# Performance work log

Measured on AMD Instinct MI355X. Metric: run time of the kernel, lower is better.

Reference implementation:

```python
import jax, jax.numpy as jnp
import numpy as np

L = 32768   # sequence length
H = 256     # dim_ssm_io
P = 128     # effective state dim = dim_ssm_state // 2 (conj_sym=True)
DT_MIN, DT_MAX = 0.001, 0.1


def setup_inputs() -> dict:
    key = jax.random.key(0)
    kB, kC, kD, kstep, ku = jax.random.split(key, 5)
    n = jnp.arange(P, dtype=jnp.float32)
    # s4d_inv initialization: Lambda = -0.5 + 1j * (P/pi) * (P/(2n+1) - 1)
    Lambda_re = -0.5 * jnp.ones((P,), dtype=jnp.float32)
    Lambda_im = (P / np.pi) * (P / (2.0 * n + 1.0) - 1.0)
    # lecun_normal over fan_in, then / sqrt(2) for conj_sym real/imag split
    B = jax.random.normal(kB, (P, H, 2), dtype=jnp.float32) / jnp.sqrt(2.0 * H)
    C = jax.random.normal(kC, (H, P, 2), dtype=jnp.float32) / jnp.sqrt(2.0 * P)
    D = jax.random.normal(kD, (H,), dtype=jnp.float32)
    log_step = (jax.random.uniform(kstep, (P,), dtype=jnp.float32)
                * (jnp.log(DT_MAX) - jnp.log(DT_MIN)) + jnp.log(DT_MIN))
    input_sequence = jax.random.normal(ku, (L, H), dtype=jnp.float32)
    return {
        "Lambda_re": Lambda_re, "Lambda_im": Lambda_im,
        "B": B, "C": C, "D": D, "log_step": log_step,
        "input_sequence": input_sequence,
    }


def reference(Lambda_re, Lambda_im, B, C, D, log_step, input_sequence):
    # assemble complex params (conj_sym path)
    Lam = Lambda_re + 1j * Lambda_im              # (P,)
    B_tilde = B[..., 0] + 1j * B[..., 1]          # (P, H)
    C_tilde = C[..., 0] + 1j * C[..., 1]          # (H, P)
    step = jnp.exp(log_step)                      # (P,)  step_rescale = 1.0
    # ZOH discretization
    Lambda_bar = jnp.exp(Lam * step)              # (P,)
    B_bar = ((Lambda_bar - 1.0) / Lam)[:, None] * B_tilde  # (P, H)
    # input projection: Bu[l] = B_bar @ u[l]
    Bu = jnp.einsum("lh,ph->lp", input_sequence.astype(B_bar.dtype), B_bar)  # (L, P)
    Lam_elems = jnp.broadcast_to(Lambda_bar, (input_sequence.shape[0], Lambda_bar.shape[0]))

    def lin_op(q_i, q_j):
        A_i, b_i = q_i
        A_j, b_j = q_j
        return (A_j * A_i, A_j * b_i + b_j)

    _, xs = jax.lax.associative_scan(lin_op, (Lam_elems, Bu))  # (L, P) complex
    # output projection with conj symmetry: 2 * Re(C_tilde @ x)
    ys = 2.0 * jnp.einsum("lp,hp->lh", xs, C_tilde).real       # (L, H)
    return ys + D * input_sequence
```

## Files before the change

### kernel.cpp

```cpp
#include <hip/hip_runtime.h>
#include <math.h>

#define L_SEQ   32768
#define H_DIM   256
#define P_DIM   128
#define P2      256
#define NBLK    512
#define ROWS    64
#define TPB     512
#define NSEG    64
#define CPS     8

#define WS_LB    0
#define WS_A64   256
#define WS_A512  512
#define WS_COEF  768
#define WS_APOW  1024
#define WS_E     17408
#define WS_CB    148480
#define WS_PACKS 279552
#define WS_XS    410624
#define WS_S     8799232
#define WS_SC    8815616

typedef __attribute__((ext_vector_type(8))) short short8;
typedef __attribute__((ext_vector_type(4))) float f32x4;

#define SAK 264
#define STL 260

__device__ __forceinline__ void split_bf16(float v, ushort& hi, ushort& lo) {
    union { float f; unsigned u; } a; a.f = v;
    unsigned r = a.u + 0x7FFFu + ((a.u >> 16) & 1u);
    hi = (ushort)(r >> 16);
    union { unsigned u; float f; } hf; hf.u = ((unsigned)hi) << 16;
    float rem = v - hf.f;
    union { float f; unsigned u; } b; b.f = rem;
    unsigned r2 = b.u + 0x7FFFu + ((b.u >> 16) & 1u);
    lo = (ushort)(r2 >> 16);
}

__device__ __forceinline__ void split_bf16_fast(float v, ushort& hi, ushort& lo) {
    union { float f; unsigned u; } a; a.f = v;
    hi = (ushort)(a.u >> 16);
    union { unsigned u; float f; } hf; hf.u = a.u & 0xFFFF0000u;
    float rem = v - hf.f;
    union { float f; unsigned u; } b; b.f = rem;
    unsigned r2 = b.u + 0x7FFFu + ((b.u >> 16) & 1u);
    lo = (ushort)(r2 >> 16);
}

__device__ __forceinline__ float4 cfma2(const float4 A, const float4 x, const float4 f) {
    float4 o;
    o.x = A.x * x.x - A.y * x.y + f.x;
    o.y = A.x * x.y + A.y * x.x + f.y;
    o.z = A.z * x.z - A.w * x.w + f.z;
    o.w = A.z * x.w + A.w * x.z + f.w;
    return o;
}

__global__ void k_setup_p(const float* __restrict__ lre, const float* __restrict__ lim,
                          const float* __restrict__ lstep, float* __restrict__ ws) {
    int p = threadIdx.x;
    if (p >= P_DIM) return;
    float step = expf(lstep[p]);
    float lr = lre[p], li = lim[p];
    double zd = (double)lr * (double)step;
    double yd = (double)li * (double)step;
    double ed = exp(zd), cd = cos(yd), sd = sin(yd);
    double lbr = ed * cd, lbi = ed * sd;
    ws[WS_LB + 2*p]     = (float)lbr;
    ws[WS_LB + 2*p + 1] = (float)lbi;
    double mr = lbr, mi = lbi;
    ws[WS_APOW + 2*p]     = (float)mr;
    ws[WS_APOW + 2*p + 1] = (float)mi;
    for (int i = 1; i < 64; i++) {
        double nr = mr * lbr - mi * lbi;
        mi = mr * lbi + mi * lbr;
        mr = nr;
        ws[WS_APOW + i*P2 + 2*p]     = (float)mr;
        ws[WS_APOW + i*P2 + 2*p + 1] = (float)mi;
    }
    ws[WS_A64 + 2*p]     = (float)mr;
    ws[WS_A64 + 2*p + 1] = (float)mi;
    double ar = mr, ai = mi;
    for (int j = 0; j < 3; j++) {
        double nr = ar*ar - ai*ai;
        ai = 2.0 * ar * ai;
        ar = nr;
    }
    ws[WS_A512 + 2*p]     = (float)ar;
    ws[WS_A512 + 2*p + 1] = (float)ai;
    float lbrf = (float)lbr, lbif = (float)lbi;
    float a = lbrf - 1.0f, b = lbif;
    float den = lr*lr + li*li;
    ws[WS_COEF + 2*p]     = (a*lr + b*li) / den;
    ws[WS_COEF + 2*p + 1] = (b*lr - a*li) / den;
}

__global__ void k_setup_mats(const float* __restrict__ B, const float* __restrict__ C,
                             const float* __restrict__ coef,
                             ushort* __restrict__ w1h, ushort* __restrict__ w1l,
                             ushort* __restrict__ w2h, ushort* __restrict__ w2l) {
    int t = blockIdx.x * blockDim.x + threadIdx.x;
    for (int e = t; e < P_DIM * H_DIM; e += 64 * 256) {
        int p = e >> 8;
        int h = e & 255;
        float br = B[(size_t)(p*H_DIM + h)*2 + 0];
        float bi = B[(size_t)(p*H_DIM + h)*2 + 1];
        float cr = coef[2*p], ci = coef[2*p + 1];
        float v1r = cr*br - ci*bi;
        float v1i = cr*bi + ci*br;
        ushort hi, lo;
        split_bf16(v1r, hi, lo);
        w1h[(size_t)(2*p)*256 + h] = hi;  w1l[(size_t)(2*p)*256 + h] = lo;
        split_bf16(v1i, hi, lo);
        w1h[(size_t)(2*p+1)*256 + h] = hi; w1l[(size_t)(2*p+1)*256 + h] = lo;
        float Cr = C[(size_t)(h*P_DIM + p)*2 + 0];
        float Ci = C[(size_t)(h*P_DIM + p)*2 + 1];
        split_bf16(2.0f*Cr, hi, lo);
        w2h[(size_t)h*256 + 2*p] = hi;    w2l[(size_t)h*256 + 2*p] = lo;
        split_bf16(-2.0f*Ci, hi, lo);
        w2h[(size_t)h*256 + 2*p+1] = hi;  w2l[(size_t)h*256 + 2*p+1] = lo;
    }
}

__global__ void k_carry_reduce(const float* __restrict__ E, float* __restrict__ S,
                               const float* __restrict__ a64) {
    const int s = blockIdx.x;
    const int q = threadIdx.x;
    const float4 A = *(const float4*)(a64 + 4 * q);
    const float* xe = E + (size_t)s * CPS * P2 + 4 * q;
    float4 e = make_float4(0.f, 0.f, 0.f, 0.f);
    #pragma unroll
    for (int j = 0; j < CPS; j++)
        e = cfma2(A, e, *(const float4*)(xe + (size_t)j * P2));
    *(float4*)(S + (size_t)s * P2 + 4 * q) = e;
}

__global__ void k_carry_scan(const float* __restrict__ S, float* __restrict__ SC,
                             const float* __restrict__ a512) {
    const int q = threadIdx.x;
    const float4 AS = *(const float4*)(a512 + 4 * q);
    float4 c = make_float4(0.f, 0.f, 0.f, 0.f);
    #pragma unroll 8
    for (int s = 0; s < NSEG; s++) {
        *(float4*)(SC + (size_t)s * P2 + 4 * q) = c;
        c = cfma2(AS, c, *(const float4*)(S + (size_t)s * P2 + 4 * q));
    }
}

__global__ void k_carry_apply(const float* __restrict__ E, const float* __restrict__ SC,
                              float* __restrict__ cb, const float* __restrict__ a64) {
    const int s = blockIdx.x;
    const int q = threadIdx.x;
    const float4 A = *(const float4*)(a64 + 4 * q);
    const float* xe = E + (size_t)s * CPS * P2 + 4 * q;
    float* cw = cb + (size_t)s * CPS * P2 + 4 * q;
    float4 c = *(const float4*)(SC + (size_t)s * P2 + 4 * q);
    #pragma unroll
    for (int j = 0; j < CPS; j++) {
        *(float4*)(cw + (size_t)j * P2) = c;
        c = cfma2(A, c, *(const float4*)(xe + (size_t)j * P2));
    }
}

template<bool EPI, bool APPLY, bool SCAN, bool BSPLIT>
__global__ __launch_bounds__(TPB, 4) void k_gemm_mfma(
        const float* __restrict__ A, const ushort* __restrict__ Wh,
        const ushort* __restrict__ Wl, float* __restrict__ Cmat,
        const float* __restrict__ Dv, const float* __restrict__ U,
        const float* __restrict__ ws, float* __restrict__ Eout,
        const float* __restrict__ cbin) {
    __shared__ float4 SMraw[4224];
    ushort* Ah   = (ushort*)SMraw;
    ushort* Al   = Ah + ROWS * SAK;
    float*  Tile = (float*)SMraw;

    const int t      = threadIdx.x;
    const int lane   = t & 63;
    const int wave   = t >> 6;
    const int lane16 = lane & 15;
    const int quad   = lane >> 4;
    const int blk    = blockIdx.x;
    const int l0     = blk * ROWS;

    {
        float4 f[8];
        #pragma unroll
        for (int j = 0; j < 8; j++)
            f[j] = *(const float4*)(A + (size_t)(l0 + j*8 + wave) * 256 + lane * 4);
        if (APPLY) {
            const float4 cr = *(const float4*)(cbin + (size_t)blk * P2 + lane * 4);
            #pragma unroll
            for (int j = 0; j < 8; j++) {
                const float4 ap = *(const float4*)(ws + WS_APOW + (size_t)(j*8 + wave) * P2 + lane * 4);
                f[j] = cfma2(ap, cr, f[j]);
            }
        }
        #pragma unroll
        for (int j = 0; j < 8; j++) {
            const int m = j*8 + wave;
            ushort4 h4, l4;
            split_bf16_fast(f[j].x, h4.x, l4.x);
            split_bf16_fast(f[j].y, h4.y, l4.y);
            split_bf16_fast(f[j].z, h4.z, l4.z);
            split_bf16_fast(f[j].w, h4.w, l4.w);
            *(ushort4*)(&Ah[m * SAK + lane * 4]) = h4;
            *(ushort4*)(&Al[m * SAK + lane * 4]) = l4;
        }
    }
    __syncthreads();

    f32x4 acc[4][2];
    #pragma unroll
    for (int i = 0; i < 4; i++)
        #pragma unroll
        for (int j = 0; j < 2; j++) acc[i][j] = (f32x4){0.f, 0.f, 0.f, 0.f};

    const ushort* WhB = Wh + (size_t)(wave * 32 + lane16) * 256 + quad * 8;
    const ushort* WlB = Wl + (size_t)(wave * 32 + lane16) * 256 + quad * 8;

    #pragma unroll
    for (int kt = 0; kt < 8; kt++) {
        const int k0 = kt * 32;
        short8 ah[4], alo[4];
        #pragma unroll
        for (int mf = 0; mf < 4; mf++) {
            int m = mf * 16 + lane16;
            ah[mf]  = *(const short8*)(&Ah[m * SAK + k0 + quad * 8]);
            alo[mf] = *(const short8*)(&Al[m * SAK + k0 + quad * 8]);
        }
        #pragma unroll
        for (int nf = 0; nf < 2; nf++) {
            short8 bh = *(const short8*)(WhB + (size_t)nf * 4096 + k0);
            short8 bl;
            if (BSPLIT) bl = *(const short8*)(WlB + (size_t)nf * 4096 + k0);
            #pragma unroll
            for (int mf = 0; mf < 4; mf++) {
                acc[mf][nf] = __builtin_amdgcn_mfma_f32_16x16x32_bf16(ah[mf],  bh, acc[mf][nf], 0, 0, 0);
                if (BSPLIT)
                    acc[mf][nf] = __builtin_amdgcn_mfma_f32_16x16x32_bf16(ah[mf], bl, acc[mf][nf], 0, 0, 0);
                acc[mf][nf] = __builtin_amdgcn_mfma_f32_16x16x32_bf16(alo[mf], bh, acc[mf][nf], 0, 0, 0);
            }
        }
    }

    __syncthreads();
    #pragma unroll
    for (int mf = 0; mf < 4; mf++)
        #pragma unroll
        for (int nf = 0; nf < 2; nf++) {
            int row = mf * 16 + quad * 4;
            int col = wave * 32 + nf * 16 + lane16;
            #pragma unroll
            for (int r = 0; r < 4; r++)
                Tile[(row + r) * STL + col] = acc[mf][nf][r];
        }
    __syncthreads();

    if (!SCAN) {
        const float4 dv = *(const float4*)(Dv + 4 * lane);
        #pragma unroll
        for (int r = 0; r < 8; r++) {
            const int row = wave * 8 + r;
            const float4 tv = *(const float4*)(Tile + row * STL + 4 * lane);
            float4 y = tv;
            if (EPI) {
                const float4 uv = *(const float4*)(U + (size_t)(l0 + row) * 256 + 4 * lane);
                y.x += dv.x * uv.x;  y.y += dv.y * uv.y;
                y.z += dv.z * uv.z;  y.w += dv.w * uv.w;
            }
            *(float4*)(Cmat + (size_t)(l0 + row) * 256 + 4 * lane) = y;
        }
    } else {
        const float4 Alb = *(const float4*)(ws + WS_LB + 4 * lane);
        const float* Trow = Tile + (wave * 8) * STL + 4 * lane;
        float4 v[8];
        float4 x = make_float4(0.f, 0.f, 0.f, 0.f);
        #pragma unroll
        for (int r = 0; r < 8; r++) {
            x = cfma2(Alb, x, *(const float4*)(Trow + r * STL));
            v[r] = x;
        }
        __syncthreads();
        *(float4*)(Tile + wave * STL + 4 * lane) = v[7];
        __syncthreads();
        if (wave == 0) {
            const float4 A8 = *(const float4*)(ws + WS_APOW + 7 * P2 + 4 * lane);
            float4 c = make_float4(0.f, 0.f, 0.f, 0.f);
            #pragma unroll
            for (int j = 0; j < 8; j++) {
                const float4 s = *(const float4*)(Tile + j * STL + 4 * lane);
                *(float4*)(Tile + (8 + j) * STL + 4 * lane) = c;
                c = cfma2(A8, c, s);
            }
        }
        __syncthreads();
        const float4 c = *(const float4*)(Tile + (8 + wave) * STL + 4 * lane);
        float* gbase = Cmat + (size_t)(l0 + wave * 8) * 256 + 4 * lane;
        #pragma unroll
        for (int r = 0; r < 8; r++) {
            const float4 ap = *(const float4*)(ws + WS_APOW + (size_t)r * P2 + 4 * lane);
            const float4 y = cfma2(ap, c, v[r]);
            *(float4*)(gbase + (size_t)r * 256) = y;
            if (r == 7 && wave == 7)
                *(float4*)(Eout + (size_t)blk * P2 + 4 * lane) = y;
        }
    }
}

extern "C" void kernel_launch(void* const* d_in, const int* in_sizes, int n_in,
                              void* d_out, int out_size, void* d_ws, size_t ws_size,
                              hipStream_t stream) {
    const float* lre   = (const float*)d_in[0];
    const float* lim   = (const float*)d_in[1];
    const float* B     = (const float*)d_in[2];
    const float* C     = (const float*)d_in[3];
    const float* D     = (const float*)d_in[4];
    const float* lstep = (const float*)d_in[5];
    const float* u     = (const float*)d_in[6];
    float* out = (float*)d_out;
    float* ws  = (float*)d_ws;
    float* xs  = ws + WS_XS;
    ushort* wpk = (ushort*)(ws + WS_PACKS);
    ushort* w1h = wpk;
    ushort* w1l = wpk + 65536;
    ushort* w2h = wpk + 131072;
    ushort* w2l = wpk + 196608;

    k_setup_p<<<1, 128, 0, stream>>>(lre, lim, lstep, ws);
    k_setup_mats<<<64, 256, 0, stream>>>(B, C, ws + WS_COEF, w1h, w1l, w2h, w2l);
    k_gemm_mfma<false, false, true, true><<<NBLK, TPB, 0, stream>>>(
        u, w1h, w1l, xs, nullptr, nullptr, ws, ws + WS_E, nullptr);
    k_carry_reduce<<<NSEG, 64, 0, stream>>>(ws + WS_E, ws + WS_S, ws + WS_A64);
    k_carry_scan<<<1, 64, 0, stream>>>(ws + WS_S, ws + WS_SC, ws + WS_A512);
    k_carry_apply<<<NSEG, 64, 0, stream>>>(ws + WS_E, ws + WS_SC, ws + WS_CB,
                                           ws + WS_A64);
    k_gemm_mfma<true, true, false, false><<<NBLK, TPB, 0, stream>>>(
        xs, w2h, w2l, out, D, u, ws, nullptr, ws + WS_CB);
}
```

Before: 149.4 us.

## Fuse both projections and the carry scan into one cooperative kernel

```diff
diff --git a/kernel.cpp b/kernel.cpp
--- a/kernel.cpp
+++ b/kernel.cpp
@@ -1,27 +1,25 @@
 #include <hip/hip_runtime.h>
+#include <hip/hip_cooperative_groups.h>
 #include <math.h>
+
+namespace cg = cooperative_groups;
 
 #define L_SEQ   32768
 #define H_DIM   256
 #define P_DIM   128
 #define P2      256
-#define NBLK    512
-#define ROWS    64
-#define TPB     512
-#define NSEG    64
-#define CPS     8
-
-#define WS_LB    0
-#define WS_A64   256
-#define WS_A512  512
-#define WS_COEF  768
-#define WS_APOW  1024
-#define WS_E     17408
-#define WS_CB    148480
-#define WS_PACKS 279552
-#define WS_XS    410624
-#define WS_S     8799232
-#define WS_SC    8815616
+#define NBLK    256
+#define ROWS    128
+#define TPB     1024
+#define NW      16
+
+#define WS_LB     0
+#define WS_APOW   256
+#define WS_A128P  33024
+#define WS_A2048  37120
+#define WS_COEF   37376
+#define WS_E      37632
+#define WS_PACKS  103168
 
 typedef __attribute__((ext_vector_type(8))) short short8;
 typedef __attribute__((ext_vector_type(4))) float f32x4;
@@ -74,23 +72,28 @@
     double mr = lbr, mi = lbi;
     ws[WS_APOW + 2*p]     = (float)mr;
     ws[WS_APOW + 2*p + 1] = (float)mi;
-    for (int i = 1; i < 64; i++) {
+    for (int i = 1; i < 128; i++) {
         double nr = mr * lbr - mi * lbi;
         mi = mr * lbi + mi * lbr;
         mr = nr;
         ws[WS_APOW + i*P2 + 2*p]     = (float)mr;
         ws[WS_APOW + i*P2 + 2*p + 1] = (float)mi;
     }
-    ws[WS_A64 + 2*p]     = (float)mr;
-    ws[WS_A64 + 2*p + 1] = (float)mi;
-    double ar = mr, ai = mi;
-    for (int j = 0; j < 3; j++) {
-        double nr = ar*ar - ai*ai;
-        ai = 2.0 * ar * ai;
+    double r128 = mr, i128 = mi;
+    double ar = 1.0, ai = 0.0;
+    ws[WS_A128P + 2*p]     = 1.0f;
+    ws[WS_A128P + 2*p + 1] = 0.0f;
+    for (int d = 1; d < 16; d++) {
+        double nr = ar * r128 - ai * i128;
+        ai = ar * i128 + ai * r128;
         ar = nr;
-    }
-    ws[WS_A512 + 2*p]     = (float)ar;
-    ws[WS_A512 + 2*p + 1] = (float)ai;
+        ws[WS_A128P + d*P2 + 2*p]     = (float)ar;
+        ws[WS_A128P + d*P2 + 2*p + 1] = (float)ai;
+    }
+    double tr = ar * r128 - ai * i128;
+    double ti = ar * i128 + ai * r128;
+    ws[WS_A2048 + 2*p]     = (float)tr;
+    ws[WS_A2048 + 2*p + 1] = (float)ti;
     float lbrf = (float)lbr, lbif = (float)lbi;
     float a = lbrf - 1.0f, b = lbif;
     float den = lr*lr + li*li;
@@ -101,7 +104,7 @@
 __global__ void k_setup_mats(const float* __restrict__ B, const float* __restrict__ C,
                              const float* __restrict__ coef,
                              ushort* __restrict__ w1h, ushort* __restrict__ w1l,
-                             ushort* __restrict__ w2h, ushort* __restrict__ w2l) {
+                             ushort* __restrict__ w2h) {
     int t = blockIdx.x * blockDim.x + threadIdx.x;
     for (int e = t; e < P_DIM * H_DIM; e += 64 * 256) {
         int p = e >> 8;
@@ -119,60 +122,18 @@
         float Cr = C[(size_t)(h*P_DIM + p)*2 + 0];
         float Ci = C[(size_t)(h*P_DIM + p)*2 + 1];
         split_bf16(2.0f*Cr, hi, lo);
-        w2h[(size_t)h*256 + 2*p] = hi;    w2l[(size_t)h*256 + 2*p] = lo;
+        w2h[(size_t)h*256 + 2*p] = hi;
         split_bf16(-2.0f*Ci, hi, lo);
-        w2h[(size_t)h*256 + 2*p+1] = hi;  w2l[(size_t)h*256 + 2*p+1] = lo;
-    }
-}
-
-__global__ void k_carry_reduce(const float* __restrict__ E, float* __restrict__ S,
-                               const float* __restrict__ a64) {
-    const int s = blockIdx.x;
-    const int q = threadIdx.x;
-    const float4 A = *(const float4*)(a64 + 4 * q);
-    const float* xe = E + (size_t)s * CPS * P2 + 4 * q;
-    float4 e = make_float4(0.f, 0.f, 0.f, 0.f);
-    #pragma unroll
-    for (int j = 0; j < CPS; j++)
-        e = cfma2(A, e, *(const float4*)(xe + (size_t)j * P2));
-    *(float4*)(S + (size_t)s * P2 + 4 * q) = e;
-}
-
-__global__ void k_carry_scan(const float* __restrict__ S, float* __restrict__ SC,
-                             const float* __restrict__ a512) {
-    const int q = threadIdx.x;
-    const float4 AS = *(const float4*)(a512 + 4 * q);
-    float4 c = make_float4(0.f, 0.f, 0.f, 0.f);
-    #pragma unroll 8
-    for (int s = 0; s < NSEG; s++) {
-        *(float4*)(SC + (size_t)s * P2 + 4 * q) = c;
-        c = cfma2(AS, c, *(const float4*)(S + (size_t)s * P2 + 4 * q));
-    }
-}
-
-__global__ void k_carry_apply(const float* __restrict__ E, const float* __restrict__ SC,
-                              float* __restrict__ cb, const float* __restrict__ a64) {
-    const int s = blockIdx.x;
-    const int q = threadIdx.x;
-    const float4 A = *(const float4*)(a64 + 4 * q);
-    const float* xe = E + (size_t)s * CPS * P2 + 4 * q;
-    float* cw = cb + (size_t)s * CPS * P2 + 4 * q;
-    float4 c = *(const float4*)(SC + (size_t)s * P2 + 4 * q);
-    #pragma unroll
-    for (int j = 0; j < CPS; j++) {
-        *(float4*)(cw + (size_t)j * P2) = c;
-        c = cfma2(A, c, *(const float4*)(xe + (size_t)j * P2));
-    }
-}
-
-template<bool EPI, bool APPLY, bool SCAN, bool BSPLIT>
-__global__ __launch_bounds__(TPB, 4) void k_gemm_mfma(
-        const float* __restrict__ A, const ushort* __restrict__ Wh,
-        const ushort* __restrict__ Wl, float* __restrict__ Cmat,
-        const float* __restrict__ Dv, const float* __restrict__ U,
-        const float* __restrict__ ws, float* __restrict__ Eout,
-        const float* __restrict__ cbin) {
-    __shared__ float4 SMraw[4224];
+        w2h[(size_t)h*256 + 2*p+1] = hi;
+    }
+}
+
+__global__ __launch_bounds__(TPB, 4) void k_fused(
+        const float* __restrict__ u, const ushort* __restrict__ w1h,
+        const ushort* __restrict__ w1l, const ushort* __restrict__ w2h,
+        float* __restrict__ out, const float* __restrict__ Dv,
+        const float* __restrict__ ws, float* __restrict__ E) {
+    __shared__ float4 SMraw[8448];
     ushort* Ah   = (ushort*)SMraw;
     ushort* Al   = Ah + ROWS * SAK;
     float*  Tile = (float*)SMraw;
@@ -189,18 +150,10 @@
         float4 f[8];
         #pragma unroll
         for (int j = 0; j < 8; j++)
-            f[j] = *(const float4*)(A + (size_t)(l0 + j*8 + wave) * 256 + lane * 4);
-        if (APPLY) {
-            const float4 cr = *(const float4*)(cbin + (size_t)blk * P2 + lane * 4);
-            #pragma unroll
-            for (int j = 0; j < 8; j++) {
-                const float4 ap = *(const float4*)(ws + WS_APOW + (size_t)(j*8 + wave) * P2 + lane * 4);
-                f[j] = cfma2(ap, cr, f[j]);
-            }
-        }
+            f[j] = *(const float4*)(u + (size_t)(l0 + j*16 + wave) * 256 + lane * 4);
         #pragma unroll
         for (int j = 0; j < 8; j++) {
-            const int m = j*8 + wave;
+            const int m = j*16 + wave;
             ushort4 h4, l4;
             split_bf16_fast(f[j].x, h4.x, l4.x);
             split_bf16_fast(f[j].y, h4.y, l4.y);
@@ -212,100 +165,175 @@
     }
     __syncthreads();
 
-    f32x4 acc[4][2];
-    #pragma unroll
-    for (int i = 0; i < 4; i++)
-        #pragma unroll
-        for (int j = 0; j < 2; j++) acc[i][j] = (f32x4){0.f, 0.f, 0.f, 0.f};
-
-    const ushort* WhB = Wh + (size_t)(wave * 32 + lane16) * 256 + quad * 8;
-    const ushort* WlB = Wl + (size_t)(wave * 32 + lane16) * 256 + quad * 8;
-
-    #pragma unroll
-    for (int kt = 0; kt < 8; kt++) {
-        const int k0 = kt * 32;
-        short8 ah[4], alo[4];
-        #pragma unroll
-        for (int mf = 0; mf < 4; mf++) {
-            int m = mf * 16 + lane16;
-            ah[mf]  = *(const short8*)(&Ah[m * SAK + k0 + quad * 8]);
-            alo[mf] = *(const short8*)(&Al[m * SAK + k0 + quad * 8]);
-        }
-        #pragma unroll
-        for (int nf = 0; nf < 2; nf++) {
-            short8 bh = *(const short8*)(WhB + (size_t)nf * 4096 + k0);
-            short8 bl;
-            if (BSPLIT) bl = *(const short8*)(WlB + (size_t)nf * 4096 + k0);
+    f32x4 acc[8];
+    #pragma unroll
+    for (int i = 0; i < 8; i++) acc[i] = (f32x4){0.f, 0.f, 0.f, 0.f};
+    {
+        const ushort* WhB = w1h + (size_t)(wave * 16 + lane16) * 256 + quad * 8;
+        const ushort* WlB = w1l + (size_t)(wave * 16 + lane16) * 256 + quad * 8;
+        #pragma unroll
+        for (int kt = 0; kt < 8; kt++) {
+            const int k0 = kt * 32;
+            short8 ah[8], alo[8];
             #pragma unroll
-            for (int mf = 0; mf < 4; mf++) {
-                acc[mf][nf] = __builtin_amdgcn_mfma_f32_16x16x32_bf16(ah[mf],  bh, acc[mf][nf], 0, 0, 0);
-                if (BSPLIT)
-                    acc[mf][nf] = __builtin_amdgcn_mfma_f32_16x16x32_bf16(ah[mf], bl, acc[mf][nf], 0, 0, 0);
-                acc[mf][nf] = __builtin_amdgcn_mfma_f32_16x16x32_bf16(alo[mf], bh, acc[mf][nf], 0, 0, 0);
-            }
-        }
-    }
-
-    __syncthreads();
-    #pragma unroll
-    for (int mf = 0; mf < 4; mf++)
-        #pragma unroll
-        for (int nf = 0; nf < 2; nf++) {
-            int row = mf * 16 + quad * 4;
-            int col = wave * 32 + nf * 16 + lane16;
+            for (int mf = 0; mf < 8; mf++) {
+                int m = mf * 16 + lane16;
+                ah[mf]  = *(const short8*)(&Ah[m * SAK + k0 + quad * 8]);
+                alo[mf] = *(const short8*)(&Al[m * SAK + k0 + quad * 8]);
+            }
+            short8 bh = *(const short8*)(WhB + k0);
+            short8 bl = *(const short8*)(WlB + k0);
             #pragma unroll
-            for (int r = 0; r < 4; r++)
-                Tile[(row + r) * STL + col] = acc[mf][nf][r];
-        }
-    __syncthreads();
-
-    if (!SCAN) {
+            for (int mf = 0; mf < 8; mf++) {
+                acc[mf] = __builtin_amdgcn_mfma_f32_16x16x32_bf16(ah[mf],  bh, acc[mf], 0, 0, 0);
+                acc[mf] = __builtin_amdgcn_mfma_f32_16x16x32_bf16(ah[mf],  bl, acc[mf], 0, 0, 0);
+                acc[mf] = __builtin_amdgcn_mfma_f32_16x16x32_bf16(alo[mf], bh, acc[mf], 0, 0, 0);
+            }
+        }
+    }
+
+    __syncthreads();
+    #pragma unroll
+    for (int mf = 0; mf < 8; mf++) {
+        int row = mf * 16 + quad * 4;
+        int col = wave * 16 + lane16;
+        #pragma unroll
+        for (int r = 0; r < 4; r++)
+            Tile[(row + r) * STL + col] = acc[mf][r];
+    }
+    __syncthreads();
+    const float4 Alb = *(const float4*)(ws + WS_LB + 4 * lane);
+    float4 v[8];
+    {
+        const float* Trow = Tile + (wave * 8) * STL + 4 * lane;
+        float4 x = make_float4(0.f, 0.f, 0.f, 0.f);
+        #pragma unroll
+        for (int r = 0; r < 8; r++) {
+            x = cfma2(Alb, x, *(const float4*)(Trow + r * STL));
+            v[r] = x;
+        }
+    }
+    __syncthreads();
+    *(float4*)(Tile + wave * STL + 4 * lane) = v[7];
+    __syncthreads();
+    if (wave == 0) {
+        const float4 A8 = *(const float4*)(ws + WS_APOW + 7 * P2 + 4 * lane);
+        float4 c = make_float4(0.f, 0.f, 0.f, 0.f);
+        #pragma unroll
+        for (int j = 0; j < 16; j++) {
+            const float4 s = *(const float4*)(Tile + j * STL + 4 * lane);
+            *(float4*)(Tile + (16 + j) * STL + 4 * lane) = c;
+            c = cfma2(A8, c, s);
+        }
+    }
+    __syncthreads();
+    {
+        const float4 cs = *(const float4*)(Tile + (16 + wave) * STL + 4 * lane);
+        #pragma unroll
+        for (int r = 0; r < 8; r++) {
+            const float4 ap = *(const float4*)(ws + WS_APOW + (size_t)r * P2 + 4 * lane);
+            v[r] = cfma2(ap, cs, v[r]);
+        }
+    }
+    if (wave == 15)
+        *(float4*)(E + (size_t)blk * P2 + 4 * lane) = v[7];
+
+    __threadfence();
+    cg::this_grid().sync();
+
+    float4 c = make_float4(0.f, 0.f, 0.f, 0.f);
+    {
+        float4 p = make_float4(0.f, 0.f, 0.f, 0.f);
+        const int cnt = (blk > wave) ? (((blk - 1 - wave) >> 4) + 1) : 0;
+        if (cnt > 0) {
+            const float4 A2 = *(const float4*)(ws + WS_A2048 + 4 * lane);
+            const float* ep = E + (size_t)wave * P2 + 4 * lane;
+            #pragma unroll 4
+            for (int m = 0; m < cnt; m++) {
+                p = cfma2(A2, p, *(const float4*)ep);
+                ep += 16 * P2;
+            }
+            const int jmax = wave + ((cnt - 1) << 4);
+            const int d = blk - 1 - jmax;
+            const float4 Ad = *(const float4*)(ws + WS_A128P + (size_t)d * P2 + 4 * lane);
+            const float4 z = make_float4(0.f, 0.f, 0.f, 0.f);
+            p = cfma2(Ad, p, z);
+        }
+        *(float4*)(Tile + wave * STL + 4 * lane) = p;
+        __syncthreads();
+        #pragma unroll
+        for (int w2 = 0; w2 < NW; w2++) {
+            const float4 q = *(const float4*)(Tile + w2 * STL + 4 * lane);
+            c.x += q.x; c.y += q.y; c.z += q.z; c.w += q.w;
+        }
+    }
+
+    #pragma unroll
+    for (int r = 0; r < 8; r++) {
+        const float4 ap = *(const float4*)(ws + WS_APOW + (size_t)(wave * 8 + r) * P2 + 4 * lane);
+        v[r] = cfma2(ap, c, v[r]);
+    }
+    __syncthreads();
+    #pragma unroll
+    for (int r = 0; r < 8; r++) {
+        const int m = wave * 8 + r;
+        ushort4 h4, l4;
+        split_bf16_fast(v[r].x, h4.x, l4.x);
+        split_bf16_fast(v[r].y, h4.y, l4.y);
+        split_bf16_fast(v[r].z, h4.z, l4.z);
+        split_bf16_fast(v[r].w, h4.w, l4.w);
+        *(ushort4*)(&Ah[m * SAK + lane * 4]) = h4;
+        *(ushort4*)(&Al[m * SAK + lane * 4]) = l4;
+    }
+    __syncthreads();
+
+    f32x4 acc2[8];
+    #pragma unroll
+    for (int i = 0; i < 8; i++) acc2[i] = (f32x4){0.f, 0.f, 0.f, 0.f};
+    {
+        const ushort* W2B = w2h + (size_t)(wave * 16 + lane16) * 256 + quad * 8;
+        #pragma unroll
+        for (int kt = 0; kt < 8; kt++) {
+            const int k0 = kt * 32;
+            short8 ah[8], alo[8];
+            #pragma unroll
+            for (int mf = 0; mf < 8; mf++) {
+                int m = mf * 16 + lane16;
+                ah[mf]  = *(const short8*)(&Ah[m * SAK + k0 + quad * 8]);
+                alo[mf] = *(const short8*)(&Al[m * SAK + k0 + quad * 8]);
+            }
+            short8 bh = *(const short8*)(W2B + k0);
+            #pragma unroll
+            for (int mf = 0; mf < 8; mf++) {
+                acc2[mf] = __builtin_amdgcn_mfma_f32_16x16x32_bf16(ah[mf],  bh, acc2[mf], 0, 0, 0);
+                acc2[mf] = __builtin_amdgcn_mfma_f32_16x16x32_bf16(alo[mf], bh, acc2[mf], 0, 0, 0);
+            }
+        }
+    }
+
+    __syncthreads();
+    #pragma unroll
+    for (int mf = 0; mf < 8; mf++) {
+        int row = mf * 16 + quad * 4;
+        int col = wave * 16 + lane16;
+        #pragma unroll
+        for (int r = 0; r < 4; r++)
+            Tile[(row + r) * STL + col] = acc2[mf][r];
+    }
+    __syncthreads();
+    {
         const float4 dv = *(const float4*)(Dv + 4 * lane);
         #pragma unroll
         for (int r = 0; r < 8; r++) {
             const int row = wave * 8 + r;
             const float4 tv = *(const float4*)(Tile + row * STL + 4 * lane);
-            float4 y = tv;
-            if (EPI) {
-                const float4 uv = *(const float4*)(U + (size_t)(l0 + row) * 256 + 4 * lane);
-                y.x += dv.x * uv.x;  y.y += dv.y * uv.y;
-                y.z += dv.z * uv.z;  y.w += dv.w * uv.w;
-            }
-            *(float4*)(Cmat + (size_t)(l0 + row) * 256 + 4 * lane) = y;
-        }
-    } else {
-        const float4 Alb = *(const float4*)(ws + WS_LB + 4 * lane);
-        const float* Trow = Tile + (wave * 8) * STL + 4 * lane;
-        float4 v[8];
-        float4 x = make_float4(0.f, 0.f, 0.f, 0.f);
-        #pragma unroll
-        for (int r = 0; r < 8; r++) {
-            x = cfma2(Alb, x, *(const float4*)(Trow + r * STL));
-            v[r] = x;
-        }
-        __syncthreads();
-        *(float4*)(Tile + wave * STL + 4 * lane) = v[7];
-        __syncthreads();
-        if (wave == 0) {
-            const float4 A8 = *(const float4*)(ws + WS_APOW + 7 * P2 + 4 * lane);
-            float4 c = make_float4(0.f, 0.f, 0.f, 0.f);
-            #pragma unroll
-            for (int j = 0; j < 8; j++) {
-                const float4 s = *(const float4*)(Tile + j * STL + 4 * lane);
-                *(float4*)(Tile + (8 + j) * STL + 4 * lane) = c;
-                c = cfma2(A8, c, s);
-            }
-        }
-        __syncthreads();
-        const float4 c = *(const float4*)(Tile + (8 + wave) * STL + 4 * lane);
-        float* gbase = Cmat + (size_t)(l0 + wave * 8) * 256 + 4 * lane;
-        #pragma unroll
-        for (int r = 0; r < 8; r++) {
-            const float4 ap = *(const float4*)(ws + WS_APOW + (size_t)r * P2 + 4 * lane);
-            const float4 y = cfma2(ap, c, v[r]);
-            *(float4*)(gbase + (size_t)r * 256) = y;
-            if (r == 7 && wave == 7)
-                *(float4*)(Eout + (size_t)blk * P2 + 4 * lane) = y;
+            const float4 uv = *(const float4*)(u + (size_t)(l0 + row) * 256 + 4 * lane);
+            float4 y;
+            y.x = tv.x + dv.x * uv.x;
+            y.y = tv.y + dv.y * uv.y;
+            y.z = tv.z + dv.z * uv.z;
+            y.w = tv.w + dv.w * uv.w;
+            *(float4*)(out + (size_t)(l0 + row) * 256 + 4 * lane) = y;
         }
     }
 }
@@ -322,21 +350,17 @@
     const float* u     = (const float*)d_in[6];
     float* out = (float*)d_out;
     float* ws  = (float*)d_ws;
-    float* xs  = ws + WS_XS;
     ushort* wpk = (ushort*)(ws + WS_PACKS);
     ushort* w1h = wpk;
     ushort* w1l = wpk + 65536;
     ushort* w2h = wpk + 131072;
-    ushort* w2l = wpk + 196608;
+    float* E = ws + WS_E;
 
     k_setup_p<<<1, 128, 0, stream>>>(lre, lim, lstep, ws);
-    k_setup_mats<<<64, 256, 0, stream>>>(B, C, ws + WS_COEF, w1h, w1l, w2h, w2l);
-    k_gemm_mfma<false, false, true, true><<<NBLK, TPB, 0, stream>>>(
-        u, w1h, w1l, xs, nullptr, nullptr, ws, ws + WS_E, nullptr);
-    k_carry_reduce<<<NSEG, 64, 0, stream>>>(ws + WS_E, ws + WS_S, ws + WS_A64);
-    k_carry_scan<<<1, 64, 0, stream>>>(ws + WS_S, ws + WS_SC, ws + WS_A512);
-    k_carry_apply<<<NSEG, 64, 0, stream>>>(ws + WS_E, ws + WS_SC, ws + WS_CB,
-                                           ws + WS_A64);
-    k_gemm_mfma<true, true, false, false><<<NBLK, TPB, 0, stream>>>(
-        xs, w2h, w2l, out, D, u, ws, nullptr, ws + WS_CB);
-}
+    k_setup_mats<<<64, 256, 0, stream>>>(B, C, ws + WS_COEF, w1h, w1l, w2h);
+
+    void* args[] = { (void*)&u, (void*)&w1h, (void*)&w1l, (void*)&w2h,
+                     (void*)&out, (void*)&D, (void*)&ws, (void*)&E };
+    hipLaunchCooperativeKernel((void*)k_fused, dim3(NBLK), dim3(TPB),
+                               args, 0, stream);
+}
```

Measured after the change: 257.7 us. +72.5%, slower.

## Double GEMM block rows to 128 with 16 waves and per-wave column slices

Applied to the files above, without the earlier changes.

```diff
diff --git a/kernel.cpp b/kernel.cpp
--- a/kernel.cpp
+++ b/kernel.cpp
@@ -5,23 +5,24 @@
 #define H_DIM   256
 #define P_DIM   128
 #define P2      256
-#define NBLK    512
-#define ROWS    64
-#define TPB     512
+#define NBLK    256
+#define ROWS    128
+#define TPB     1024
+#define NW      16
 #define NSEG    64
-#define CPS     8
+#define CPS     4
 
 #define WS_LB    0
-#define WS_A64   256
+#define WS_A128  256
 #define WS_A512  512
 #define WS_COEF  768
 #define WS_APOW  1024
-#define WS_E     17408
-#define WS_CB    148480
-#define WS_PACKS 279552
-#define WS_XS    410624
-#define WS_S     8799232
-#define WS_SC    8815616
+#define WS_E     33792
+#define WS_CB    99328
+#define WS_PACKS 164864
+#define WS_XS    295936
+#define WS_S     8684544
+#define WS_SC    8700928
 
 typedef __attribute__((ext_vector_type(8))) short short8;
 typedef __attribute__((ext_vector_type(4))) float f32x4;
@@ -74,17 +75,17 @@
     double mr = lbr, mi = lbi;
     ws[WS_APOW + 2*p]     = (float)mr;
     ws[WS_APOW + 2*p + 1] = (float)mi;
-    for (int i = 1; i < 64; i++) {
+    for (int i = 1; i < 128; i++) {
         double nr = mr * lbr - mi * lbi;
         mi = mr * lbi + mi * lbr;
         mr = nr;
         ws[WS_APOW + i*P2 + 2*p]     = (float)mr;
         ws[WS_APOW + i*P2 + 2*p + 1] = (float)mi;
     }
-    ws[WS_A64 + 2*p]     = (float)mr;
-    ws[WS_A64 + 2*p + 1] = (float)mi;
+    ws[WS_A128 + 2*p]     = (float)mr;
+    ws[WS_A128 + 2*p + 1] = (float)mi;
     double ar = mr, ai = mi;
-    for (int j = 0; j < 3; j++) {
+    for (int j = 0; j < 2; j++) {
         double nr = ar*ar - ai*ai;
         ai = 2.0 * ar * ai;
         ar = nr;
@@ -101,7 +102,7 @@
 __global__ void k_setup_mats(const float* __restrict__ B, const float* __restrict__ C,
                              const float* __restrict__ coef,
                              ushort* __restrict__ w1h, ushort* __restrict__ w1l,
-                             ushort* __restrict__ w2h, ushort* __restrict__ w2l) {
+                             ushort* __restrict__ w2h) {
     int t = blockIdx.x * blockDim.x + threadIdx.x;
     for (int e = t; e < P_DIM * H_DIM; e += 64 * 256) {
         int p = e >> 8;
@@ -119,17 +120,17 @@
         float Cr = C[(size_t)(h*P_DIM + p)*2 + 0];
         float Ci = C[(size_t)(h*P_DIM + p)*2 + 1];
         split_bf16(2.0f*Cr, hi, lo);
-        w2h[(size_t)h*256 + 2*p] = hi;    w2l[(size_t)h*256 + 2*p] = lo;
+        w2h[(size_t)h*256 + 2*p] = hi;
         split_bf16(-2.0f*Ci, hi, lo);
-        w2h[(size_t)h*256 + 2*p+1] = hi;  w2l[(size_t)h*256 + 2*p+1] = lo;
+        w2h[(size_t)h*256 + 2*p+1] = hi;
     }
 }
 
 __global__ void k_carry_reduce(const float* __restrict__ E, float* __restrict__ S,
-                               const float* __restrict__ a64) {
+                               const float* __restrict__ a128) {
     const int s = blockIdx.x;
     const int q = threadIdx.x;
-    const float4 A = *(const float4*)(a64 + 4 * q);
+    const float4 A = *(const float4*)(a128 + 4 * q);
     const float* xe = E + (size_t)s * CPS * P2 + 4 * q;
     float4 e = make_float4(0.f, 0.f, 0.f, 0.f);
     #pragma unroll
@@ -151,10 +152,10 @@
 }
 
 __global__ void k_carry_apply(const float* __restrict__ E, const float* __restrict__ SC,
-                              float* __restrict__ cb, const float* __restrict__ a64) {
+                              float* __restrict__ cb, const float* __restrict__ a128) {
     const int s = blockIdx.x;
     const int q = threadIdx.x;
-    const float4 A = *(const float4*)(a64 + 4 * q);
+    const float4 A = *(const float4*)(a128 + 4 * q);
     const float* xe = E + (size_t)s * CPS * P2 + 4 * q;
     float* cw = cb + (size_t)s * CPS * P2 + 4 * q;
     float4 c = *(const float4*)(SC + (size_t)s * P2 + 4 * q);
@@ -172,7 +173,7 @@
         const float* __restrict__ Dv, const float* __restrict__ U,
         const float* __restrict__ ws, float* __restrict__ Eout,
         const float* __restrict__ cbin) {
-    __shared__ float4 SMraw[4224];
+    __shared__ float4 SMraw[8448];
     ushort* Ah   = (ushort*)SMraw;
     ushort* Al   = Ah + ROWS * SAK;
     float*  Tile = (float*)SMraw;
@@ -189,18 +190,18 @@
         float4 f[8];
         #pragma unroll
         for (int j = 0; j < 8; j++)
-            f[j] = *(const float4*)(A + (size_t)(l0 + j*8 + wave) * 256 + lane * 4);
+            f[j] = *(const float4*)(A + (size_t)(l0 + j*16 + wave) * 256 + lane * 4);
         if (APPLY) {
             const float4 cr = *(const float4*)(cbin + (size_t)blk * P2 + lane * 4);
             #pragma unroll
             for (int j = 0; j < 8; j++) {
-                const float4 ap = *(const float4*)(ws + WS_APOW + (size_t)(j*8 + wave) * P2 + lane * 4);
+                const float4 ap = *(const float4*)(ws + WS_APOW + (size_t)(j*16 + wave) * P2 + lane * 4);
                 f[j] = cfma2(ap, cr, f[j]);
             }
         }
         #pragma unroll
         for (int j = 0; j < 8; j++) {
-            const int m = j*8 + wave;
+            const int m = j*16 + wave;
             ushort4 h4, l4;
             split_bf16_fast(f[j].x, h4.x, l4.x);
             split_bf16_fast(f[j].y, h4.y, l4.y);
@@ -212,51 +213,40 @@
     }
     __syncthreads();
 
-    f32x4 acc[4][2];
-    #pragma unroll
-    for (int i = 0; i < 4; i++)
-        #pragma unroll
-        for (int j = 0; j < 2; j++) acc[i][j] = (f32x4){0.f, 0.f, 0.f, 0.f};
-
-    const ushort* WhB = Wh + (size_t)(wave * 32 + lane16) * 256 + quad * 8;
-    const ushort* WlB = Wl + (size_t)(wave * 32 + lane16) * 256 + quad * 8;
+    f32x4 acc[8];
+    #pragma unroll
+    for (int i = 0; i < 8; i++) acc[i] = (f32x4){0.f, 0.f, 0.f, 0.f};
+
+    const ushort* WhB = Wh + (size_t)(wave * 16 + lane16) * 256 + quad * 8;
+    const ushort* WlB = Wl + (size_t)(wave * 16 + lane16) * 256 + quad * 8;
 
     #pragma unroll
     for (int kt = 0; kt < 8; kt++) {
         const int k0 = kt * 32;
-        short8 ah[4], alo[4];
-        #pragma unroll
-        for (int mf = 0; mf < 4; mf++) {
-            int m = mf * 16 + lane16;
-            ah[mf]  = *(const short8*)(&Ah[m * SAK + k0 + quad * 8]);
-            alo[mf] = *(const short8*)(&Al[m * SAK + k0 + quad * 8]);
-        }
-        #pragma unroll
-        for (int nf = 0; nf < 2; nf++) {
-            short8 bh = *(const short8*)(WhB + (size_t)nf * 4096 + k0);
-            short8 bl;
-            if (BSPLIT) bl = *(const short8*)(WlB + (size_t)nf * 4096 + k0);
-            #pragma unroll
-            for (int mf = 0; mf < 4; mf++) {
-                acc[mf][nf] = __builtin_amdgcn_mfma_f32_16x16x32_bf16(ah[mf],  bh, acc[mf][nf], 0, 0, 0);
-                if (BSPLIT)
-                    acc[mf][nf] = __builtin_amdgcn_mfma_f32_16x16x32_bf16(ah[mf], bl, acc[mf][nf], 0, 0, 0);
-                acc[mf][nf] = __builtin_amdgcn_mfma_f32_16x16x32_bf16(alo[mf], bh, acc[mf][nf], 0, 0, 0);
-            }
+        short8 bh = *(const short8*)(WhB + k0);
+        short8 bl;
+        if (BSPLIT) bl = *(const short8*)(WlB + k0);
+        #pragma unroll
+        for (int mf = 0; mf < 8; mf++) {
+            const int m = mf * 16 + lane16;
+            short8 ah  = *(const short8*)(&Ah[m * SAK + k0 + quad * 8]);
+            short8 alo = *(const short8*)(&Al[m * SAK + k0 + quad * 8]);
+            acc[mf] = __builtin_amdgcn_mfma_f32_16x16x32_bf16(ah,  bh, acc[mf], 0, 0, 0);
+            if (BSPLIT)
+                acc[mf] = __builtin_amdgcn_mfma_f32_16x16x32_bf16(ah, bl, acc[mf], 0, 0, 0);
+            acc[mf] = __builtin_amdgcn_mfma_f32_16x16x32_bf16(alo, bh, acc[mf], 0, 0, 0);
         }
     }
 
     __syncthreads();
     #pragma unroll
-    for (int mf = 0; mf < 4; mf++)
-        #pragma unroll
-        for (int nf = 0; nf < 2; nf++) {
-            int row = mf * 16 + quad * 4;
-            int col = wave * 32 + nf * 16 + lane16;
-            #pragma unroll
-            for (int r = 0; r < 4; r++)
-                Tile[(row + r) * STL + col] = acc[mf][nf][r];
-        }
+    for (int mf = 0; mf < 8; mf++) {
+        int row = mf * 16 + quad * 4;
+        int col = wave * 16 + lane16;
+        #pragma unroll
+        for (int r = 0; r < 4; r++)
+            Tile[(row + r) * STL + col] = acc[mf][r];
+    }
     __syncthreads();
 
     if (!SCAN) {
@@ -275,13 +265,15 @@
         }
     } else {
         const float4 Alb = *(const float4*)(ws + WS_LB + 4 * lane);
-        const float* Trow = Tile + (wave * 8) * STL + 4 * lane;
         float4 v[8];
-        float4 x = make_float4(0.f, 0.f, 0.f, 0.f);
-        #pragma unroll
-        for (int r = 0; r < 8; r++) {
-            x = cfma2(Alb, x, *(const float4*)(Trow + r * STL));
-            v[r] = x;
+        {
+            const float* Trow = Tile + (wave * 8) * STL + 4 * lane;
+            float4 x = make_float4(0.f, 0.f, 0.f, 0.f);
+            #pragma unroll
+            for (int r = 0; r < 8; r++) {
+                x = cfma2(Alb, x, *(const float4*)(Trow + r * STL));
+                v[r] = x;
+            }
         }
         __syncthreads();
         *(float4*)(Tile + wave * STL + 4 * lane) = v[7];
@@ -290,21 +282,21 @@
             const float4 A8 = *(const float4*)(ws + WS_APOW + 7 * P2 + 4 * lane);
             float4 c = make_float4(0.f, 0.f, 0.f, 0.f);
             #pragma unroll
-            for (int j = 0; j < 8; j++) {
+            for (int j = 0; j < 16; j++) {
                 const float4 s = *(const float4*)(Tile + j * STL + 4 * lane);
-                *(float4*)(Tile + (8 + j) * STL + 4 * lane) = c;
+                *(float4*)(Tile + (16 + j) * STL + 4 * lane) = c;
                 c = cfma2(A8, c, s);
             }
         }
         __syncthreads();
-        const float4 c = *(const float4*)(Tile + (8 + wave) * STL + 4 * lane);
+        const float4 cs = *(const float4*)(Tile + (16 + wave) * STL + 4 * lane);
         float* gbase = Cmat + (size_t)(l0 + wave * 8) * 256 + 4 * lane;
         #pragma unroll
         for (int r = 0; r < 8; r++) {
             const float4 ap = *(const float4*)(ws + WS_APOW + (size_t)r * P2 + 4 * lane);
-            const float4 y = cfma2(ap, c, v[r]);
+            const float4 y = cfma2(ap, cs, v[r]);
             *(float4*)(gbase + (size_t)r * 256) = y;
-            if (r == 7 && wave == 7)
+            if (r == 7 && wave == 15)
                 *(float4*)(Eout + (size_t)blk * P2 + 4 * lane) = y;
         }
     }
@@ -327,16 +319,15 @@
     ushort* w1h = wpk;
     ushort* w1l = wpk + 65536;
     ushort* w2h = wpk + 131072;
-    ushort* w2l = wpk + 196608;
 
     k_setup_p<<<1, 128, 0, stream>>>(lre, lim, lstep, ws);
-    k_setup_mats<<<64, 256, 0, stream>>>(B, C, ws + WS_COEF, w1h, w1l, w2h, w2l);
+    k_setup_mats<<<64, 256, 0, stream>>>(B, C, ws + WS_COEF, w1h, w1l, w2h);
     k_gemm_mfma<false, false, true, true><<<NBLK, TPB, 0, stream>>>(
         u, w1h, w1l, xs, nullptr, nullptr, ws, ws + WS_E, nullptr);
-    k_carry_reduce<<<NSEG, 64, 0, stream>>>(ws + WS_E, ws + WS_S, ws + WS_A64);
+    k_carry_reduce<<<NSEG, 64, 0, stream>>>(ws + WS_E, ws + WS_S, ws + WS_A128);
     k_carry_scan<<<1, 64, 0, stream>>>(ws + WS_S, ws + WS_SC, ws + WS_A512);
     k_carry_apply<<<NSEG, 64, 0, stream>>>(ws + WS_E, ws + WS_SC, ws + WS_CB,
-                                           ws + WS_A64);
+                                           ws + WS_A128);
     k_gemm_mfma<true, true, false, false><<<NBLK, TPB, 0, stream>>>(
-        xs, w2h, w2l, out, D, u, ws, nullptr, ws + WS_CB);
-}
+        xs, w2h, nullptr, out, D, u, ws, nullptr, ws + WS_CB);
+}
```

Measured after the change: 151.8 us. Within noise of the previous version (+1.6%).
